# Kernel tuning notes

Hardware: AMD Instinct MI355X
Metric: run time of the kernel (lower is better)

Reference implementation:

```python
import jax, jax.numpy as jnp
import numpy as np

H, KV, HD = 32, 8, 128
EPS = 1e-6
THETA = 10000.0


def _rmsnorm(x, w):
    # RMSNorm over last dim (head_dim), per Qwen3 per-head q/k norm
    var = jnp.mean(jnp.square(x), axis=-1, keepdims=True)
    return x * jax.lax.rsqrt(var + EPS) * w


def _rope(x, cos, sin):
    # NeoX-style rotary: split head_dim into two halves
    x1, x2 = jnp.split(x, 2, axis=-1)
    return jnp.concatenate([x1 * cos - x2 * sin, x2 * cos + x1 * sin], axis=-1)


def setup_inputs() -> dict:
    key = jax.random.key(0)
    k1, k2, k3 = jax.random.split(key, 3)
    B, S, D = 2, 2048, 4096
    positions = jnp.broadcast_to(jnp.arange(S, dtype=jnp.int32), (B, S))
    hidden_states = jax.random.normal(k1, (B, S, D), dtype=jnp.float32)
    w_qkv = jax.random.normal(k2, (D, (H + 2 * KV) * HD), dtype=jnp.float32) * (D ** -0.5)
    w_o = jax.random.normal(k3, (H * HD, D), dtype=jnp.float32) * ((H * HD) ** -0.5)
    q_norm_w = jnp.ones((HD,), dtype=jnp.float32)
    k_norm_w = jnp.ones((HD,), dtype=jnp.float32)
    return {"positions": positions, "hidden_states": hidden_states,
            "w_qkv": w_qkv, "w_o": w_o, "q_norm_w": q_norm_w, "k_norm_w": k_norm_w}


def reference(positions, hidden_states, w_qkv, w_o, q_norm_w, k_norm_w):
    B, S, D = hidden_states.shape
    scale = HD ** -0.5
    G = H // KV  # query heads per kv head

    qkv = hidden_states @ w_qkv  # [B,S,(H+2KV)*HD]
    q, k, v = jnp.split(qkv, [H * HD, (H + KV) * HD], axis=-1)
    q = q.reshape(B, S, H, HD)
    k = k.reshape(B, S, KV, HD)
    v = v.reshape(B, S, KV, HD)

    # per-head RMSNorm on q and k
    q = _rmsnorm(q, q_norm_w)
    k = _rmsnorm(k, k_norm_w)

    # RoPE
    inv_freq = 1.0 / (THETA ** (jnp.arange(0, HD, 2, dtype=jnp.float32) / HD))  # [HD/2]
    ang = positions.astype(jnp.float32)[..., None] * inv_freq  # [B,S,HD/2]
    cos = jnp.cos(ang)[:, :, None, :]  # [B,S,1,HD/2]
    sin = jnp.sin(ang)[:, :, None, :]
    q = _rope(q, cos, sin)
    k = _rope(k, cos, sin)

    # causal GQA attention
    qg = q.reshape(B, S, KV, G, HD)
    scores = jnp.einsum('bskgd,btkd->bkgst', qg, k) * scale  # [B,KV,G,S,S]
    causal = jnp.tril(jnp.ones((S, S), dtype=bool))
    scores = jnp.where(causal, scores, jnp.finfo(scores.dtype).min)
    probs = jax.nn.softmax(scores, axis=-1)
    o = jnp.einsum('bkgst,btkd->bskgd', probs, v).reshape(B, S, H * HD)

    return o @ w_o  # [B,S,D]
```

## Files before the change

kernel.cpp:

```cpp
#include <hip/hip_runtime.h>
#include <hip/hip_bf16.h>


#define S_LEN   2048
#define DMODEL  4096
#define NHEAD   32
#define NKV     8
#define HDIM    128
#define QKV_N   6144
#define QKV_STRIDE 5120
#define ATT_SCALE 0.08838834764831843f
#define FP32_ONES_WORD 0x3F800000u

typedef unsigned short ushort_t;
typedef unsigned int   uint_t;
typedef __attribute__((ext_vector_type(8))) short bf16x8;
typedef __attribute__((ext_vector_type(4))) float f32x4;

__device__ __forceinline__ float bflo(uint_t u) { return __uint_as_float(u << 16); }
__device__ __forceinline__ float bfhi(uint_t u) { return __uint_as_float(u & 0xffff0000u); }
__device__ __forceinline__ float bf2f(ushort_t u) { return __uint_as_float(((uint_t)u) << 16); }
__device__ __forceinline__ ushort_t f2bf(float f) {
    uint_t u = __float_as_uint(f);
    u += 0x7fffu + ((u >> 16) & 1u);
    return (ushort_t)(u >> 16);
}
__device__ __forceinline__ void unpack8(uint4 w, float* f) {
    f[0] = bflo(w.x); f[1] = bfhi(w.x);
    f[2] = bflo(w.y); f[3] = bfhi(w.y);
    f[4] = bflo(w.z); f[5] = bfhi(w.z);
    f[6] = bflo(w.w); f[7] = bfhi(w.w);
}
union V8 { uint4 v; ushort_t u[8]; };
union U4 { uint2 v; ushort_t u[4]; };

__device__ __forceinline__ V8 load8_dual(const void* base, size_t idx, bool fp32) {
    V8 r;
    if (fp32) {
        const float* p = (const float*)base + idx;
        const float4 a = *(const float4*)p;
        const float4 b = *(const float4*)(p + 4);
        r.u[0] = f2bf(a.x); r.u[1] = f2bf(a.y); r.u[2] = f2bf(a.z); r.u[3] = f2bf(a.w);
        r.u[4] = f2bf(b.x); r.u[5] = f2bf(b.y); r.u[6] = f2bf(b.z); r.u[7] = f2bf(b.w);
    } else {
        r.v = *(const uint4*)((const ushort_t*)base + idx);
    }
    return r;
}

__device__ __forceinline__ void gload_lds16(const ushort_t* g, ushort_t* l) {
    __builtin_amdgcn_global_load_lds(
        (const __attribute__((address_space(1))) void*)g,
        (__attribute__((address_space(3))) void*)l, 16, 0, 0);
}

__global__ __launch_bounds__(256) void gemm_mfma(
    const ushort_t* __restrict__ A, const ushort_t* __restrict__ BT,
    void* __restrict__ C, size_t c_off, int M, int N, int K, int ldc,
    ushort_t* __restrict__ vT, int v_split,
    const uint_t* __restrict__ probe, int c_dual) {
    __shared__ ushort_t As[128 * 32];
    __shared__ ushort_t Bs[128 * 32];

    const int t = threadIdx.x;
    const int w = t >> 6, lane = t & 63;
    const int wr = w >> 1, wc = w & 1;
    const int m16 = lane & 15, quad = lane >> 4;
    const int m0 = blockIdx.y * 128, n0 = blockIdx.x * 128;

    f32x4 acc[4][4];
#pragma unroll
    for (int i = 0; i < 4; ++i)
#pragma unroll
        for (int j = 0; j < 4; ++j) acc[i][j] = (f32x4){0.f, 0.f, 0.f, 0.f};

    const int sm = t >> 2;
    const int kk = (t & 3) * 8;
    const ushort_t* ag0 = A  + (size_t)(m0 + sm) * K + kk;
    const ushort_t* ag1 = A  + (size_t)(m0 + 64 + sm) * K + kk;
    const ushort_t* bg0 = BT + (size_t)(n0 + sm) * K + kk;
    const ushort_t* bg1 = BT + (size_t)(n0 + 64 + sm) * K + kk;
    ushort_t* al0 = &As[w * 512];
    ushort_t* al1 = &As[2048 + w * 512];
    ushort_t* bl0 = &Bs[w * 512];
    ushort_t* bl1 = &Bs[2048 + w * 512];

    for (int kt = 0; kt < K; kt += 32) {
        __syncthreads();
        gload_lds16(ag0 + kt, al0);
        gload_lds16(ag1 + kt, al1);
        gload_lds16(bg0 + kt, bl0);
        gload_lds16(bg1 + kt, bl1);
        __syncthreads();

        bf16x8 af[4], bfr[4];
#pragma unroll
        for (int i = 0; i < 4; ++i)
            af[i] = *(const bf16x8*)&As[(wr * 64 + i * 16 + m16) * 32 + quad * 8];
#pragma unroll
        for (int j = 0; j < 4; ++j)
            bfr[j] = *(const bf16x8*)&Bs[(wc * 64 + j * 16 + m16) * 32 + quad * 8];
#pragma unroll
        for (int i = 0; i < 4; ++i)
#pragma unroll
            for (int j = 0; j < 4; ++j)
                acc[i][j] = __builtin_amdgcn_mfma_f32_16x16x32_bf16(
                    af[i], bfr[j], acc[i][j], 0, 0, 0);
    }

    const bool cf = c_dual && (probe[0] == FP32_ONES_WORD);
    if (cf) {
        float* Cf = (float*)C + c_off;
#pragma unroll
        for (int i = 0; i < 4; ++i) {
            const int row0 = m0 + wr * 64 + i * 16 + quad * 4;
#pragma unroll
            for (int j = 0; j < 4; ++j) {
                const int col = n0 + wc * 64 + j * 16 + m16;
#pragma unroll
                for (int r = 0; r < 4; ++r)
                    Cf[(size_t)(row0 + r) * ldc + col] = acc[i][j][r];
            }
        }
    } else if (v_split && n0 >= QKV_STRIDE) {
#pragma unroll
        for (int i = 0; i < 4; ++i) {
            const int row0 = m0 + wr * 64 + i * 16 + quad * 4;
#pragma unroll
            for (int j = 0; j < 4; ++j) {
                const int col = n0 + wc * 64 + j * 16 + m16;
                ushort_t* vp = vT + (size_t)(col - QKV_STRIDE) * S_LEN + row0;
#pragma unroll
                for (int r = 0; r < 4; ++r) vp[r] = f2bf(acc[i][j][r]);
            }
        }
    } else {
        ushort_t* Cb = (ushort_t*)C + c_off;
#pragma unroll
        for (int i = 0; i < 4; ++i) {
            const int row0 = m0 + wr * 64 + i * 16 + quad * 4;
#pragma unroll
            for (int j = 0; j < 4; ++j) {
                const int col = n0 + wc * 64 + j * 16 + m16;
#pragma unroll
                for (int r = 0; r < 4; ++r)
                    Cb[(size_t)(row0 + r) * ldc + col] = f2bf(acc[i][j][r]);
            }
        }
    }
}

__global__ __launch_bounds__(256) void transpose_cvt(
    const void* __restrict__ B, ushort_t* __restrict__ BT,
    int K, int N, const uint_t* __restrict__ probe) {
    const bool f32 = (probe[0] == FP32_ONES_WORD);
    __shared__ ushort_t tile[64][68];
    const int t = threadIdx.x, tx = t & 15, ty = t >> 4;
    const int n0 = blockIdx.x * 64, k0 = blockIdx.y * 64;

#pragma unroll
    for (int i = 0; i < 4; ++i) {
        const int k = ty + 16 * i;
        U4 v;
        if (f32) {
            const float4 f = *(const float4*)((const float*)B + (size_t)(k0 + k) * N + n0 + tx * 4);
            v.u[0] = f2bf(f.x); v.u[1] = f2bf(f.y); v.u[2] = f2bf(f.z); v.u[3] = f2bf(f.w);
        } else {
            v.v = *(const uint2*)((const ushort_t*)B + (size_t)(k0 + k) * N + n0 + tx * 4);
        }
        *(uint2*)&tile[k][tx * 4] = v.v;
    }
    __syncthreads();
#pragma unroll
    for (int i = 0; i < 4; ++i) {
        const int n = ty + 16 * i;
        const int k = tx * 4;
        U4 v;
        v.u[0] = tile[k][n]; v.u[1] = tile[k + 1][n];
        v.u[2] = tile[k + 2][n]; v.u[3] = tile[k + 3][n];
        *(uint2*)&BT[(size_t)(n0 + n) * K + k0 + k] = v.v;
    }
}

__global__ __launch_bounds__(256) void cvt_bf16(
    const void* __restrict__ src, size_t s_off, ushort_t* __restrict__ dst,
    const uint_t* __restrict__ probe) {
    const bool f32 = (probe[0] == FP32_ONES_WORD);
    const size_t i4 = ((size_t)blockIdx.x * 256 + threadIdx.x) * 4;
    if (f32) {
        const float4 f = *(const float4*)((const float*)src + s_off + i4);
        U4 v;
        v.u[0] = f2bf(f.x); v.u[1] = f2bf(f.y); v.u[2] = f2bf(f.z); v.u[3] = f2bf(f.w);
        *(uint2*)(dst + i4) = v.v;
    } else {
        *(uint2*)(dst + i4) = *(const uint2*)((const ushort_t*)src + s_off + i4);
    }
}

__global__ __launch_bounds__(256) void qk_norm_rope(
    ushort_t* __restrict__ qkv_b, const int* __restrict__ pos_b,
    const void* __restrict__ qw, const void* __restrict__ kw,
    const uint_t* __restrict__ probe, int stride) {
    const bool fp32 = (probe[0] == FP32_ONES_WORD);
    const int hh = blockIdx.x * 4 + (threadIdx.x >> 6);
    const int s  = blockIdx.y;
    const int t  = threadIdx.x & 63;
    ushort_t* p = qkv_b + (size_t)s * stride + hh * HDIM;

    float x1 = bf2f(p[t]);
    float x2 = bf2f(p[t + 64]);
    float ss = x1 * x1 + x2 * x2;
#pragma unroll
    for (int off = 32; off; off >>= 1) ss += __shfl_xor(ss, off);
    const float inv = rsqrtf(ss * (1.0f / 128.0f) + 1e-6f);

    const void* w = (hh < NHEAD) ? qw : kw;
    const float w1 = fp32 ? ((const float*)w)[t]      : bf2f(((const ushort_t*)w)[t]);
    const float w2 = fp32 ? ((const float*)w)[t + 64] : bf2f(((const ushort_t*)w)[t + 64]);
    const float n1 = x1 * inv * w1;
    const float n2 = x2 * inv * w2;

    const float pos  = (float)pos_b[s];
    const float freq = __expf((float)t * (-9.210340371976184f / 64.0f));
    float sv, cv;
    sincosf(pos * freq, &sv, &cv);

    p[t]      = f2bf(n1 * cv - n2 * sv);
    p[t + 64] = f2bf(n2 * cv + n1 * sv);
}

__global__ __launch_bounds__(256) void flash_attn_mfma(
    const ushort_t* __restrict__ qkv_b, const ushort_t* __restrict__ vT_b,
    ushort_t* __restrict__ o_b) {
    __shared__ ushort_t Ks[2][64 * 128];
    __shared__ ushort_t Vt[128 * 64];
    __shared__ ushort_t Ps[64 * 72];

    const int lin = blockIdx.x;
    const int L = (lin & 7) * 64 + (lin >> 3);
    const int hk = L >> 6;
    const int rem = L & 63;
    const int h = hk * 4 + (rem >> 4);
    const int pr = rem & 15;

    const int t = threadIdx.x, w = t >> 6;
    const int lane = t & 63, m16 = lane & 15, quad = lane >> 4;

    const ushort_t* kbase = qkv_b + DMODEL + hk * HDIM;
    const ushort_t* vbase = vT_b + (size_t)(hk * HDIM) * S_LEN;

    const int kkey_l = t >> 4;
    const int kcol   = (t & 15) * 8;
    const int vdim_l = t >> 3;
    const int vcol   = (t & 7) * 8;

    auto stage_k = [&](int kt, int buf) {
#pragma unroll
        for (int i = 0; i < 4; ++i) {
            const int key = i * 16 + kkey_l;
            const ushort_t* src = kbase + (size_t)(kt * 64 + key) * QKV_STRIDE
                                + (kcol ^ ((key & 7) << 3));
            gload_lds16(src, &Ks[buf][i * 2048 + t * 8]);
        }
    };
    auto stage_v = [&](int kt) {
#pragma unroll
        for (int i = 0; i < 4; ++i) {
            const int dim = i * 32 + vdim_l;
            const ushort_t* src = vbase + (size_t)dim * S_LEN + kt * 64
                                + (vcol ^ ((dim & 7) << 3));
            gload_lds16(src, &Vt[i * 2048 + t * 8]);
        }
    };

    stage_k(0, 0);
    int cur = 0;

    const int swz = (m16 & 7) << 3;

    for (int seg = 0; seg < 2; ++seg) {
        const int qt = seg ? (31 - pr) : pr;
        const int q0 = qt * 64;

        bf16x8 qf[4];
        {
            const ushort_t* qrow = qkv_b + (size_t)(q0 + w * 16 + m16) * QKV_STRIDE
                                 + h * HDIM + quad * 8;
#pragma unroll
            for (int c = 0; c < 4; ++c) qf[c] = *(const bf16x8*)(qrow + 32 * c);
        }

        f32x4 acc_o[8];
#pragma unroll
        for (int nt = 0; nt < 8; ++nt) acc_o[nt] = (f32x4){0.f, 0.f, 0.f, 0.f};
        float m_ln = -1e30f, l_ln = 0.f;
        const int qg = q0 + w * 16 + m16;

        for (int kt = 0; kt <= qt; ++kt) {
            stage_v(kt);
            __syncthreads();

            f32x4 sc[4];
#pragma unroll
            for (int jt = 0; jt < 4; ++jt) sc[jt] = (f32x4){0.f, 0.f, 0.f, 0.f};
            __builtin_amdgcn_s_setprio(1);
#pragma unroll
            for (int c = 0; c < 4; ++c) {
#pragma unroll
                for (int jt = 0; jt < 4; ++jt) {
                    const bf16x8 kf = *(const bf16x8*)
                        &Ks[cur][(((jt * 16 + m16) << 7) + 32 * c + quad * 8) ^ swz];
                    sc[jt] = __builtin_amdgcn_mfma_f32_16x16x32_bf16(kf, qf[c], sc[jt], 0, 0, 0);
                }
            }
            __builtin_amdgcn_s_setprio(0);

            const int nkt = (kt < qt) ? kt + 1 : 0;
            stage_k(nkt, cur ^ 1);

            const bool diag = (kt == qt);
            float mloc = -1e30f;
#pragma unroll
            for (int jt = 0; jt < 4; ++jt)
#pragma unroll
                for (int r = 0; r < 4; ++r) {
                    float s = sc[jt][r] * ATT_SCALE;
                    if (diag && (kt * 64 + jt * 16 + quad * 4 + r) > qg) s = -1e30f;
                    sc[jt][r] = s;
                    mloc = fmaxf(mloc, s);
                }
            mloc = fmaxf(mloc, __shfl_xor(mloc, 16));
            mloc = fmaxf(mloc, __shfl_xor(mloc, 32));
            const float mnew = fmaxf(m_ln, mloc);

            float ls = 0.f;
#pragma unroll
            for (int jt = 0; jt < 4; ++jt) {
                U4 pk;
#pragma unroll
                for (int r = 0; r < 4; ++r) {
                    const float p = __expf(sc[jt][r] - mnew);
                    ls += p;
                    pk.u[r] = f2bf(p);
                }
                *(uint2*)&Ps[(w * 16 + m16) * 72 + jt * 16 + quad * 4] = pk.v;
            }
            const float alpha = __expf(m_ln - mnew);
            m_ln = mnew;
            float lsr = ls + __shfl_xor(ls, 16);
            lsr += __shfl_xor(lsr, 32);
            l_ln = l_ln * alpha + lsr;

            float alpha_r[4];
#pragma unroll
            for (int r = 0; r < 4; ++r) alpha_r[r] = __shfl(alpha, quad * 4 + r);
#pragma unroll
            for (int nt = 0; nt < 8; ++nt)
#pragma unroll
                for (int r = 0; r < 4; ++r) acc_o[nt][r] *= alpha_r[r];

            __builtin_amdgcn_s_setprio(1);
#pragma unroll
            for (int kc = 0; kc < 2; ++kc) {
                const bf16x8 pf = *(const bf16x8*)&Ps[(w * 16 + m16) * 72 + kc * 32 + quad * 8];
#pragma unroll
                for (int nt = 0; nt < 8; ++nt) {
                    const bf16x8 vf = *(const bf16x8*)
                        &Vt[(((nt * 16 + m16) << 6) + kc * 32 + quad * 8) ^ swz];
                    acc_o[nt] = __builtin_amdgcn_mfma_f32_16x16x32_bf16(pf, vf, acc_o[nt], 0, 0, 0);
                }
            }
            __builtin_amdgcn_s_setprio(0);

            __syncthreads();
            cur ^= 1;
        }

        float invl[4];
#pragma unroll
        for (int r = 0; r < 4; ++r) invl[r] = 1.0f / __shfl(l_ln, quad * 4 + r);
#pragma unroll
        for (int nt = 0; nt < 8; ++nt) {
#pragma unroll
            for (int r = 0; r < 4; ++r) {
                const int row = q0 + w * 16 + quad * 4 + r;
                o_b[(size_t)row * DMODEL + h * HDIM + nt * 16 + m16] = f2bf(acc_o[nt][r] * invl[r]);
            }
        }
    }
}

__global__ __launch_bounds__(256) void gemm_dual(
    const void* __restrict__ A, size_t a_off,
    const void* __restrict__ B,
    void* __restrict__ C, size_t c_off,
    int M, int N, int K,
    const uint_t* __restrict__ probe, int a_dual, int b_dual, int c_dual) {
    const bool fp32 = (probe[0] == FP32_ONES_WORD);
    const bool af = a_dual && fp32;
    const bool bfl = b_dual && fp32;
    const bool cf = c_dual && fp32;

    __shared__ ushort_t As[16][136];
    __shared__ ushort_t Bs[16][136];

    const int t  = threadIdx.x;
    const int tx = t & 15, ty = t >> 4;
    const int m0 = blockIdx.y * 128, n0 = blockIdx.x * 128;

    float acc[8][8];
#pragma unroll
    for (int i = 0; i < 8; ++i)
#pragma unroll
        for (int j = 0; j < 8; ++j) acc[i][j] = 0.f;

    const int a_row = t >> 1, a_kc = (t & 1) * 8;
    const int b_row = t >> 4, b_nc = (t & 15) * 8;

    for (int k0 = 0; k0 < K; k0 += 16) {
        const size_t ai = a_off + (size_t)(m0 + a_row) * K + (a_kc + k0);
        const size_t bi = (size_t)(b_row + k0) * N + (n0 + b_nc);
        V8 av = load8_dual(A, ai, af);
        V8 bv = load8_dual(B, bi, bfl);
        __syncthreads();
#pragma unroll
        for (int q = 0; q < 8; ++q) As[a_kc + q][a_row] = av.u[q];
        *(uint4*)&Bs[b_row][b_nc] = bv.v;
        __syncthreads();

#pragma unroll
        for (int kk = 0; kk < 16; ++kk) {
            float a[8], b[8];
            unpack8(*(const uint4*)&As[kk][ty * 8], a);
            unpack8(*(const uint4*)&Bs[kk][tx * 8], b);
#pragma unroll
            for (int i = 0; i < 8; ++i)
#pragma unroll
                for (int j = 0; j < 8; ++j) acc[i][j] += a[i] * b[j];
        }
    }

    if (cf) {
        float* Cf = (float*)C + c_off;
#pragma unroll
        for (int i = 0; i < 8; ++i) {
            const size_t row = m0 + ty * 8 + i;
            float* p = Cf + row * N + n0 + tx * 8;
            *(float4*)p       = make_float4(acc[i][0], acc[i][1], acc[i][2], acc[i][3]);
            *(float4*)(p + 4) = make_float4(acc[i][4], acc[i][5], acc[i][6], acc[i][7]);
        }
    } else {
        ushort_t* Cb = (ushort_t*)C + c_off;
#pragma unroll
        for (int i = 0; i < 8; ++i) {
            const size_t row = m0 + ty * 8 + i;
            V8 ob;
#pragma unroll
            for (int j = 0; j < 8; ++j) ob.u[j] = f2bf(acc[i][j]);
            *(uint4*)(Cb + row * N + n0 + tx * 8) = ob.v;
        }
    }
}

__global__ __launch_bounds__(256) void flash_attn(
    const ushort_t* __restrict__ qkv_b, ushort_t* __restrict__ o_b) {
    __shared__ ushort_t Qs[64][136];
    __shared__ ushort_t KsT[64][136];
    __shared__ ushort_t Vs[64][136];
    __shared__ ushort_t Pw[64][68];
    __shared__ float row_m[64];
    __shared__ float row_l[64];

    const int qt = blockIdx.x, h = blockIdx.y;
    const int q0 = qt * 64;
    const int hk = h >> 2;
    const int t  = threadIdx.x;
    const int tx = t & 15, ty = t >> 4;

    {
        const ushort_t* qbase = qkv_b + (size_t)q0 * QKV_N + h * HDIM;
#pragma unroll
        for (int q = 0; q < 4; ++q) {
            const int lin = q * 256 + t;
            const int r = lin >> 4, c = (lin & 15) * 8;
            *(uint4*)&Qs[r][c] = *(const uint4*)(qbase + (size_t)r * QKV_N + c);
        }
    }
    if (t < 64) { row_m[t] = -1e30f; row_l[t] = 0.f; }

    float oacc[4][8];
#pragma unroll
    for (int i = 0; i < 4; ++i)
#pragma unroll
        for (int d = 0; d < 8; ++d) oacc[i][d] = 0.f;

    const ushort_t* kbase0 = qkv_b + (NHEAD + hk) * HDIM;
    const ushort_t* vbase0 = qkv_b + (NHEAD + NKV + hk) * HDIM;

    for (int kt = 0; kt <= qt; ++kt) {
        __syncthreads();
        {
            const ushort_t* kb = kbase0 + (size_t)(kt * 64) * QKV_N;
            const ushort_t* vb = vbase0 + (size_t)(kt * 64) * QKV_N;
#pragma unroll
            for (int q = 0; q < 4; ++q) {
                const int lin = q * 256 + t;
                const int r = lin >> 4, c = (lin & 15) * 8;
                *(uint4*)&KsT[r][c] = *(const uint4*)(kb + (size_t)r * QKV_N + c);
                *(uint4*)&Vs[r][c] = *(const uint4*)(vb + (size_t)r * QKV_N + c);
            }
        }
        __syncthreads();

        float sc[4][4];
#pragma unroll
        for (int i = 0; i < 4; ++i)
#pragma unroll
            for (int j = 0; j < 4; ++j) sc[i][j] = 0.f;

        for (int d0 = 0; d0 < HDIM; d0 += 8) {
            float qa[4][8], kb_[4][8];
#pragma unroll
            for (int i = 0; i < 4; ++i) unpack8(*(const uint4*)&Qs[ty * 4 + i][d0], qa[i]);
#pragma unroll
            for (int j = 0; j < 4; ++j) unpack8(*(const uint4*)&KsT[tx + 16 * j][d0], kb_[j]);
#pragma unroll
            for (int i = 0; i < 4; ++i)
#pragma unroll
                for (int j = 0; j < 4; ++j)
#pragma unroll
                    for (int d = 0; d < 8; ++d) sc[i][j] += qa[i][d] * kb_[j][d];
        }

        float alpha_arr[4];
#pragma unroll
        for (int i = 0; i < 4; ++i) {
            const int r  = ty * 4 + i;
            const int qg = q0 + r;
            float mloc = -1e30f;
#pragma unroll
            for (int j = 0; j < 4; ++j) {
                const int kg = kt * 64 + tx + 16 * j;
                float s = sc[i][j] * ATT_SCALE;
                if (kg > qg) s = -1e30f;
                sc[i][j] = s;
                mloc = fmaxf(mloc, s);
            }
#pragma unroll
            for (int off = 1; off < 16; off <<= 1)
                mloc = fmaxf(mloc, __shfl_xor(mloc, off));
            const float mold = row_m[r];
            const float mnew = fmaxf(mold, mloc);
            float ls = 0.f;
#pragma unroll
            for (int j = 0; j < 4; ++j) {
                const float p = __expf(sc[i][j] - mnew);
                ls += p;
                Pw[r][tx + 16 * j] = f2bf(p);
            }
#pragma unroll
            for (int off = 1; off < 16; off <<= 1)
                ls += __shfl_xor(ls, off);
            const float alpha = __expf(mold - mnew);
            if (tx == 0) { row_m[r] = mnew; row_l[r] = row_l[r] * alpha + ls; }
            alpha_arr[i] = alpha;
        }

#pragma unroll
        for (int i = 0; i < 4; ++i)
#pragma unroll
            for (int d = 0; d < 8; ++d) oacc[i][d] *= alpha_arr[i];

        for (int j0 = 0; j0 < 64; j0 += 2) {
            float px[4], py[4];
#pragma unroll
            for (int i = 0; i < 4; ++i) {
                const uint_t wv = *(const uint_t*)&Pw[ty * 4 + i][j0];
                px[i] = bflo(wv); py[i] = bfhi(wv);
            }
            float va[8], vb_[8];
            unpack8(*(const uint4*)&Vs[j0][tx * 8], va);
            unpack8(*(const uint4*)&Vs[j0 + 1][tx * 8], vb_);
#pragma unroll
            for (int i = 0; i < 4; ++i)
#pragma unroll
                for (int d = 0; d < 8; ++d)
                    oacc[i][d] += px[i] * va[d] + py[i] * vb_[d];
        }
    }

#pragma unroll
    for (int i = 0; i < 4; ++i) {
        const int r = ty * 4 + i;
        const float inv = 1.0f / row_l[r];
        V8 ob;
#pragma unroll
        for (int d = 0; d < 8; ++d) ob.u[d] = f2bf(oacc[i][d] * inv);
        *(uint4*)(o_b + (size_t)(q0 + r) * (NHEAD * HDIM) + h * HDIM + tx * 8) = ob.v;
    }
}

extern "C" void kernel_launch(void* const* d_in, const int* in_sizes, int n_in,
                              void* d_out, int out_size, void* d_ws, size_t ws_size,
                              hipStream_t stream) {
    const int*    positions = (const int*)d_in[0];
    const void*   hs        = d_in[1];
    const void*   w_qkv     = d_in[2];
    const void*   w_o       = d_in[3];
    const void*   qw        = d_in[4];
    const void*   kw        = d_in[5];
    const uint_t* probe     = (const uint_t*)d_in[4];

    const size_t SZ_WQKVT = (size_t)QKV_N * DMODEL;
    const size_t SZ_WOT   = (size_t)DMODEL * DMODEL;
    const size_t SZ_QKV   = (size_t)S_LEN * QKV_STRIDE;
    const size_t SZ_VT    = (size_t)(NKV * HDIM) * S_LEN;
    const size_t SZ_X     = (size_t)S_LEN * DMODEL;
    const size_t TIER1 = (SZ_WQKVT + SZ_WOT + SZ_QKV + SZ_VT + SZ_X) * 2;
    const size_t TIER2 = (SZ_WQKVT + SZ_QKV + SZ_VT + SZ_X) * 2;

    if (ws_size >= TIER1) {
        ushort_t* wqkvT = (ushort_t*)d_ws;
        ushort_t* woT   = wqkvT + SZ_WQKVT;
        ushort_t* qkv_b = woT + SZ_WOT;
        ushort_t* vT    = qkv_b + SZ_QKV;
        ushort_t* X     = vT + SZ_VT;

        transpose_cvt<<<dim3(QKV_N / 64, DMODEL / 64), 256, 0, stream>>>(
            w_qkv, wqkvT, DMODEL, QKV_N, probe);
        transpose_cvt<<<dim3(DMODEL / 64, DMODEL / 64), 256, 0, stream>>>(
            w_o, woT, DMODEL, DMODEL, probe);

        for (int b = 0; b < 2; ++b) {
            const size_t tok_off = (size_t)b * S_LEN;
            cvt_bf16<<<(int)(SZ_X / 1024), 256, 0, stream>>>(
                hs, tok_off * DMODEL, X, probe);
            gemm_mfma<<<dim3(QKV_N / 128, S_LEN / 128), 256, 0, stream>>>(
                X, wqkvT, qkv_b, 0, S_LEN, QKV_N, DMODEL, QKV_STRIDE,
                vT, 1, probe, 0);
            qk_norm_rope<<<dim3((NHEAD + NKV) / 4, S_LEN), 256, 0, stream>>>(
                qkv_b, positions + tok_off, qw, kw, probe, QKV_STRIDE);
            flash_attn_mfma<<<dim3(512), 256, 0, stream>>>(
                qkv_b, vT, X);
            gemm_mfma<<<dim3(DMODEL / 128, S_LEN / 128), 256, 0, stream>>>(
                X, woT, d_out, tok_off * DMODEL, S_LEN, DMODEL, DMODEL, DMODEL,
                nullptr, 0, probe, 1);
        }
    } else if (ws_size >= TIER2) {
        ushort_t* wT    = (ushort_t*)d_ws;
        ushort_t* qkv_b = wT + SZ_WQKVT;
        ushort_t* vT    = qkv_b + SZ_QKV;
        ushort_t* X     = vT + SZ_VT;

        for (int b = 0; b < 2; ++b) {
            const size_t tok_off = (size_t)b * S_LEN;
            transpose_cvt<<<dim3(QKV_N / 64, DMODEL / 64), 256, 0, stream>>>(
                w_qkv, wT, DMODEL, QKV_N, probe);
            cvt_bf16<<<(int)(SZ_X / 1024), 256, 0, stream>>>(
                hs, tok_off * DMODEL, X, probe);
            gemm_mfma<<<dim3(QKV_N / 128, S_LEN / 128), 256, 0, stream>>>(
                X, wT, qkv_b, 0, S_LEN, QKV_N, DMODEL, QKV_STRIDE,
                vT, 1, probe, 0);
            qk_norm_rope<<<dim3((NHEAD + NKV) / 4, S_LEN), 256, 0, stream>>>(
                qkv_b, positions + tok_off, qw, kw, probe, QKV_STRIDE);
            flash_attn_mfma<<<dim3(512), 256, 0, stream>>>(
                qkv_b, vT, X);
            transpose_cvt<<<dim3(DMODEL / 64, DMODEL / 64), 256, 0, stream>>>(
                w_o, wT, DMODEL, DMODEL, probe);
            gemm_mfma<<<dim3(DMODEL / 128, S_LEN / 128), 256, 0, stream>>>(
                X, wT, d_out, tok_off * DMODEL, S_LEN, DMODEL, DMODEL, DMODEL,
                nullptr, 0, probe, 1);
        }
    } else {
        ushort_t* qkv_b  = (ushort_t*)d_ws;
        ushort_t* obuf_b = qkv_b + (size_t)S_LEN * QKV_N;

        for (int b = 0; b < 2; ++b) {
            const size_t tok_off = (size_t)b * S_LEN;
            gemm_dual<<<dim3(QKV_N / 128, S_LEN / 128), 256, 0, stream>>>(
                hs, tok_off * DMODEL, w_qkv, qkv_b, 0, S_LEN, QKV_N, DMODEL,
                probe, 1, 1, 0);
            qk_norm_rope<<<dim3((NHEAD + NKV) / 4, S_LEN), 256, 0, stream>>>(
                qkv_b, positions + tok_off, qw, kw, probe, QKV_N);
            flash_attn<<<dim3(S_LEN / 64, NHEAD), 256, 0, stream>>>(qkv_b, obuf_b);
            gemm_dual<<<dim3(DMODEL / 128, S_LEN / 128), 256, 0, stream>>>(
                obuf_b, 0, w_o, d_out, tok_off * DMODEL, S_LEN, DMODEL, DMODEL,
                probe, 0, 1, 1);
        }
    }
}
```

Before: 930.6 us.

## Replace 128x128 GEMM with double-buffered swizzled 256x256 tile kernel

```diff
diff --git a/kernel.cpp b/kernel.cpp
--- a/kernel.cpp
+++ b/kernel.cpp
@@ -54,69 +54,101 @@
         (__attribute__((address_space(3))) void*)l, 16, 0, 0);
 }
 
-__global__ __launch_bounds__(256) void gemm_mfma(
+__global__ __launch_bounds__(512) void gemm_256(
     const ushort_t* __restrict__ A, const ushort_t* __restrict__ BT,
     void* __restrict__ C, size_t c_off, int M, int N, int K, int ldc,
     ushort_t* __restrict__ vT, int v_split,
     const uint_t* __restrict__ probe, int c_dual) {
-    __shared__ ushort_t As[128 * 32];
-    __shared__ ushort_t Bs[128 * 32];
+    __shared__ ushort_t As[2][256 * 64];
+    __shared__ ushort_t Bs[2][256 * 64];
 
     const int t = threadIdx.x;
     const int w = t >> 6, lane = t & 63;
-    const int wr = w >> 1, wc = w & 1;
+    const int wm = w >> 2, wn = w & 3;
     const int m16 = lane & 15, quad = lane >> 4;
-    const int m0 = blockIdx.y * 128, n0 = blockIdx.x * 128;
-
-    f32x4 acc[4][4];
-#pragma unroll
-    for (int i = 0; i < 4; ++i)
+    const int n0 = blockIdx.x * 256, m0 = blockIdx.y * 256;
+
+    f32x4 acc[8][4];
+#pragma unroll
+    for (int i = 0; i < 8; ++i)
 #pragma unroll
         for (int j = 0; j < 4; ++j) acc[i][j] = (f32x4){0.f, 0.f, 0.f, 0.f};
 
-    const int sm = t >> 2;
-    const int kk = (t & 3) * 8;
-    const ushort_t* ag0 = A  + (size_t)(m0 + sm) * K + kk;
-    const ushort_t* ag1 = A  + (size_t)(m0 + 64 + sm) * K + kk;
-    const ushort_t* bg0 = BT + (size_t)(n0 + sm) * K + kk;
-    const ushort_t* bg1 = BT + (size_t)(n0 + 64 + sm) * K + kk;
-    ushort_t* al0 = &As[w * 512];
-    ushort_t* al1 = &As[2048 + w * 512];
-    ushort_t* bl0 = &Bs[w * 512];
-    ushort_t* bl1 = &Bs[2048 + w * 512];
-
-    for (int kt = 0; kt < K; kt += 32) {
+    const int srow0  = t >> 3;
+    const int scol16 = t & 7;
+    const ushort_t* agp[4];
+    const ushort_t* bgp[4];
+#pragma unroll
+    for (int e = 0; e < 4; ++e) {
+        const int row = e * 64 + srow0;
+        const int col = (scol16 ^ (row & 7)) * 8;
+        agp[e] = A  + (size_t)(m0 + row) * K + col;
+        bgp[e] = BT + (size_t)(n0 + row) * K + col;
+    }
+
+    auto stage = [&](int buf, int kt) {
+        const int ko = kt * 64;
+#pragma unroll
+        for (int e = 0; e < 4; ++e)
+            gload_lds16(agp[e] + ko, &As[buf][(e * 512 + t) * 8]);
+#pragma unroll
+        for (int e = 0; e < 4; ++e)
+            gload_lds16(bgp[e] + ko, &Bs[buf][(e * 512 + t) * 8]);
+    };
+
+    const int rswz = (m16 & 7) << 3;
+
+    stage(0, 0);
+    __syncthreads();
+    int cur = 0;
+    const int nk = K >> 6;
+
+    for (int kt = 0; kt < nk; ++kt) {
+        bf16x8 bfrag[4][2];
+#pragma unroll
+        for (int j = 0; j < 4; ++j)
+#pragma unroll
+            for (int k2 = 0; k2 < 2; ++k2)
+                bfrag[j][k2] = *(const bf16x8*)
+                    &Bs[cur][(((wn * 64 + j * 16 + m16) << 6) + k2 * 32 + quad * 8) ^ rswz];
+
+        if (kt + 1 < nk) stage(cur ^ 1, kt + 1);
+
+#pragma unroll
+        for (int p = 0; p < 4; ++p) {
+            bf16x8 afrag[2][2];
+#pragma unroll
+            for (int ii = 0; ii < 2; ++ii)
+#pragma unroll
+                for (int k2 = 0; k2 < 2; ++k2)
+                    afrag[ii][k2] = *(const bf16x8*)
+                        &As[cur][(((wm * 128 + (p * 2 + ii) * 16 + m16) << 6)
+                                  + k2 * 32 + quad * 8) ^ rswz];
+            __builtin_amdgcn_s_setprio(1);
+#pragma unroll
+            for (int ii = 0; ii < 2; ++ii)
+#pragma unroll
+                for (int j = 0; j < 4; ++j)
+#pragma unroll
+                    for (int k2 = 0; k2 < 2; ++k2)
+                        acc[p * 2 + ii][j] = __builtin_amdgcn_mfma_f32_16x16x32_bf16(
+                            afrag[ii][k2], bfrag[j][k2], acc[p * 2 + ii][j], 0, 0, 0);
+            __builtin_amdgcn_s_setprio(0);
+        }
+
         __syncthreads();
-        gload_lds16(ag0 + kt, al0);
-        gload_lds16(ag1 + kt, al1);
-        gload_lds16(bg0 + kt, bl0);
-        gload_lds16(bg1 + kt, bl1);
-        __syncthreads();
-
-        bf16x8 af[4], bfr[4];
-#pragma unroll
-        for (int i = 0; i < 4; ++i)
-            af[i] = *(const bf16x8*)&As[(wr * 64 + i * 16 + m16) * 32 + quad * 8];
-#pragma unroll
-        for (int j = 0; j < 4; ++j)
-            bfr[j] = *(const bf16x8*)&Bs[(wc * 64 + j * 16 + m16) * 32 + quad * 8];
-#pragma unroll
-        for (int i = 0; i < 4; ++i)
-#pragma unroll
-            for (int j = 0; j < 4; ++j)
-                acc[i][j] = __builtin_amdgcn_mfma_f32_16x16x32_bf16(
-                    af[i], bfr[j], acc[i][j], 0, 0, 0);
+        cur ^= 1;
     }
 
     const bool cf = c_dual && (probe[0] == FP32_ONES_WORD);
     if (cf) {
         float* Cf = (float*)C + c_off;
 #pragma unroll
-        for (int i = 0; i < 4; ++i) {
-            const int row0 = m0 + wr * 64 + i * 16 + quad * 4;
+        for (int i = 0; i < 8; ++i) {
+            const int row0 = m0 + wm * 128 + i * 16 + quad * 4;
 #pragma unroll
             for (int j = 0; j < 4; ++j) {
-                const int col = n0 + wc * 64 + j * 16 + m16;
+                const int col = n0 + wn * 64 + j * 16 + m16;
 #pragma unroll
                 for (int r = 0; r < 4; ++r)
                     Cf[(size_t)(row0 + r) * ldc + col] = acc[i][j][r];
@@ -124,11 +156,11 @@
         }
     } else if (v_split && n0 >= QKV_STRIDE) {
 #pragma unroll
-        for (int i = 0; i < 4; ++i) {
-            const int row0 = m0 + wr * 64 + i * 16 + quad * 4;
+        for (int i = 0; i < 8; ++i) {
+            const int row0 = m0 + wm * 128 + i * 16 + quad * 4;
 #pragma unroll
             for (int j = 0; j < 4; ++j) {
-                const int col = n0 + wc * 64 + j * 16 + m16;
+                const int col = n0 + wn * 64 + j * 16 + m16;
                 ushort_t* vp = vT + (size_t)(col - QKV_STRIDE) * S_LEN + row0;
 #pragma unroll
                 for (int r = 0; r < 4; ++r) vp[r] = f2bf(acc[i][j][r]);
@@ -137,11 +169,11 @@
     } else {
         ushort_t* Cb = (ushort_t*)C + c_off;
 #pragma unroll
-        for (int i = 0; i < 4; ++i) {
-            const int row0 = m0 + wr * 64 + i * 16 + quad * 4;
+        for (int i = 0; i < 8; ++i) {
+            const int row0 = m0 + wm * 128 + i * 16 + quad * 4;
 #pragma unroll
             for (int j = 0; j < 4; ++j) {
-                const int col = n0 + wc * 64 + j * 16 + m16;
+                const int col = n0 + wn * 64 + j * 16 + m16;
 #pragma unroll
                 for (int r = 0; r < 4; ++r)
                     Cb[(size_t)(row0 + r) * ldc + col] = f2bf(acc[i][j][r]);
@@ -635,14 +667,14 @@
             const size_t tok_off = (size_t)b * S_LEN;
             cvt_bf16<<<(int)(SZ_X / 1024), 256, 0, stream>>>(
                 hs, tok_off * DMODEL, X, probe);
-            gemm_mfma<<<dim3(QKV_N / 128, S_LEN / 128), 256, 0, stream>>>(
+            gemm_256<<<dim3(QKV_N / 256, S_LEN / 256), 512, 0, stream>>>(
                 X, wqkvT, qkv_b, 0, S_LEN, QKV_N, DMODEL, QKV_STRIDE,
                 vT, 1, probe, 0);
             qk_norm_rope<<<dim3((NHEAD + NKV) / 4, S_LEN), 256, 0, stream>>>(
                 qkv_b, positions + tok_off, qw, kw, probe, QKV_STRIDE);
             flash_attn_mfma<<<dim3(512), 256, 0, stream>>>(
                 qkv_b, vT, X);
-            gemm_mfma<<<dim3(DMODEL / 128, S_LEN / 128), 256, 0, stream>>>(
+            gemm_256<<<dim3(DMODEL / 256, S_LEN / 256), 512, 0, stream>>>(
                 X, woT, d_out, tok_off * DMODEL, S_LEN, DMODEL, DMODEL, DMODEL,
                 nullptr, 0, probe, 1);
         }
@@ -658,7 +690,7 @@
                 w_qkv, wT, DMODEL, QKV_N, probe);
             cvt_bf16<<<(int)(SZ_X / 1024), 256, 0, stream>>>(
                 hs, tok_off * DMODEL, X, probe);
-            gemm_mfma<<<dim3(QKV_N / 128, S_LEN / 128), 256, 0, stream>>>(
+            gemm_256<<<dim3(QKV_N / 256, S_LEN / 256), 512, 0, stream>>>(
                 X, wT, qkv_b, 0, S_LEN, QKV_N, DMODEL, QKV_STRIDE,
                 vT, 1, probe, 0);
             qk_norm_rope<<<dim3((NHEAD + NKV) / 4, S_LEN), 256, 0, stream>>>(
@@ -667,7 +699,7 @@
                 qkv_b, vT, X);
             transpose_cvt<<<dim3(DMODEL / 64, DMODEL / 64), 256, 0, stream>>>(
                 w_o, wT, DMODEL, DMODEL, probe);
-            gemm_mfma<<<dim3(DMODEL / 128, S_LEN / 128), 256, 0, stream>>>(
+            gemm_256<<<dim3(DMODEL / 256, S_LEN / 256), 512, 0, stream>>>(
                 X, wT, d_out, tok_off * DMODEL, S_LEN, DMODEL, DMODEL, DMODEL,
                 nullptr, 0, probe, 1);
         }
```

After: 858.8 us. -7.7%, faster.
